# Kernel tuning notes

Measured on AMD Instinct MI355X. Metric: run time of the kernel, lower is better.

The kernel has to match this reference:

```python
import jax, jax.numpy as jnp
from jax import lax
import numpy as np

N, C, T, V, P, O = 32, 64, 300, 25, 3, 128
STRIDE = 2
EPS = 1e-5


def setup_inputs() -> dict:
    key = jax.random.key(0)
    ks = jax.random.split(key, 8)
    x = jax.random.normal(ks[0], (N, C, T, V), jnp.float32)
    A_parts = jax.random.uniform(ks[1], (P, V, V), jnp.float32)
    edge_importance = jnp.ones((P,), jnp.float32)
    gcn_w = jax.random.normal(ks[2], (O, C), jnp.float32) * 0.05
    gcn_b = jax.random.normal(ks[3], (O,), jnp.float32) * 0.05
    tcn_w = jax.random.normal(ks[4], (O, O, 9, 1), jnp.float32) * 0.02
    tcn_b = jax.random.normal(ks[5], (O,), jnp.float32) * 0.05
    bn_gamma = jnp.ones((O,), jnp.float32)
    bn_beta = jnp.zeros((O,), jnp.float32)
    res_w = jax.random.normal(ks[6], (O, C), jnp.float32) * 0.05
    res_b = jax.random.normal(ks[7], (O,), jnp.float32) * 0.05
    return {"x": x, "A_parts": A_parts, "edge_importance": edge_importance,
            "gcn_w": gcn_w, "gcn_b": gcn_b, "tcn_w": tcn_w, "tcn_b": tcn_b,
            "bn_gamma": bn_gamma, "bn_beta": bn_beta, "res_w": res_w, "res_b": res_b}


def reference(x, A_parts, edge_importance, gcn_w, gcn_b, tcn_w, tcn_b,
              bn_gamma, bn_beta, res_w, res_b):
    # Fused P-partition aggregation: sum_p (ei_p * A_p) applied once.
    A_sum = jnp.einsum('pvw,p->vw', A_parts, edge_importance)  # [V, V]
    agg = jnp.einsum('nctv,vw->nctw', x, A_sum)                # [N, C, T, V]
    # 1x1 gcn conv == channel matmul
    x_gcn = jnp.einsum('nctv,oc->notv', agg, gcn_w) + gcn_b[None, :, None, None]
    # temporal conv: kernel (9,1), stride (2,1), pad (4,0)
    x_tcn = lax.conv_general_dilated(
        x_gcn, tcn_w, window_strides=(STRIDE, 1), padding=((4, 4), (0, 0)),
        dimension_numbers=('NCHW', 'OIHW', 'NCHW'))
    x_tcn = x_tcn + tcn_b[None, :, None, None]
    # BatchNorm (training mode: batch statistics, biased variance)
    mean = jnp.mean(x_tcn, axis=(0, 2, 3), keepdims=True)
    var = jnp.var(x_tcn, axis=(0, 2, 3), keepdims=True)
    x_bn = (x_tcn - mean) * lax.rsqrt(var + EPS)
    x_bn = x_bn * bn_gamma[None, :, None, None] + bn_beta[None, :, None, None]
    # residual: 1x1 conv, stride (2,1) == temporal subsample + channel matmul
    x_sub = x[:, :, ::STRIDE, :]
    res = jnp.einsum('nctv,oc->notv', x_sub, res_w) + res_b[None, :, None, None]
    return jax.nn.relu(x_bn + res)
```

## Files before the change

kernel.cpp:

```cpp
#include <hip/hip_runtime.h>
#include <hip/hip_bf16.h>

typedef unsigned short u16;
typedef unsigned int   u32;

#define NB 32
#define CC 64
#define TT 300
#define VV 25
#define OO 128
#define TO 150
#define KT 9
#define MM 7500
#define MT 59
#define M2 3750

typedef short s8v  __attribute__((ext_vector_type(8)));
typedef float f4v  __attribute__((ext_vector_type(4)));
typedef u16  h4v  __attribute__((ext_vector_type(4)));
typedef u16  h8v  __attribute__((ext_vector_type(8)));

__device__ __forceinline__ float b2f(u16 u){
  union { u32 i; float f; } c; c.i = ((u32)u) << 16; return c.f;
}
__device__ __forceinline__ u16 f2b(float f){
  __hip_bfloat16 h = __float2bfloat16(f);
  return *reinterpret_cast<u16*>(&h);
}
__device__ __forceinline__ void async16(const void* g, void* l){
  __builtin_amdgcn_global_load_lds((const __attribute__((address_space(1))) u32*)g,
                                   (__attribute__((address_space(3))) u32*)l, 16, 0, 0);
}

__global__ __launch_bounds__(256) void k_prep(const float* __restrict__ Ap, const float* __restrict__ ei,
                                              const float* __restrict__ tw, const float* __restrict__ gw,
                                              const float* __restrict__ rw,
                                              float* __restrict__ Asum, float* __restrict__ zbuf,
                                              u16* __restrict__ Wq2, u16* __restrict__ gwb,
                                              u16* __restrict__ rwb){
  int idx = blockIdx.x * 256 + threadIdx.x;
  if (idx < VV*VV){
    float s = 0.f;
    for (int p = 0; p < 3; ++p) s += ei[p] * Ap[p*VV*VV + idx];
    Asum[idx] = s;
  }
  if (idx >= 640 && idx < 768) zbuf[idx - 640] = 0.f;
  int w = idx - 1024;
  if (w >= 0 && w < 18*OO*64){
    int kc = w >> 13;
    int r  = w & 8191;
    int o  = r >> 6;
    int j  = r & 63;
    int k  = kc >> 1;
    int i  = (kc & 1)*64 + j;
    Wq2[w] = f2b(tw[o*(OO*KT) + i*KT + k]);
  }
  int w2 = idx - 148480;
  if (w2 >= 0 && w2 < OO*CC) gwb[w2] = f2b(gw[w2]);
  int w3 = idx - 156672;
  if (w3 >= 0 && w3 < OO*CC) rwb[w3] = f2b(rw[w3]);
}

__global__ __launch_bounds__(256, 4) void k_gcnm(const float* __restrict__ x, const float* __restrict__ Asum,
                                                 const u16* __restrict__ gwb, const float* __restrict__ gb,
                                                 u16* __restrict__ xg){
  __shared__ __align__(16) u16 A_lds[128*64];
  __shared__ __align__(16) u16 B_lds[128*64];
  int bx = blockIdx.x;
  int n  = bx / MT;
  int m0 = (bx % MT) * 128;
  int t0 = m0 / VV, r0 = m0 % VV;
  int tid = threadIdx.x;
  int lane = tid & 63, wv = tid >> 6;
  int wm = (wv & 1) * 64, wo = (wv >> 1) * 64;
  int lr = lane & 15, lq = lane >> 4;

  {
    const u32* g32 = (const u32*)gwb;
    u32* b32 = (u32*)B_lds;
    for (int s = tid; s < 4096; s += 256){
      int row = s >> 5, col = s & 31;
      int g = col >> 2, c2 = col & 3;
      b32[row*32 + ((g ^ (row & 7))*4 + c2)] = g32[s];
    }
  }

  s8v bfw[2];
  #pragma unroll
  for (int wt = 0; wt < 2; ++wt){
    u16 tmp[8];
    int w = lr + 16*wt;
    #pragma unroll
    for (int j = 0; j < 8; ++j){
      int v = lq*8 + j;
      tmp[j] = (w < VV && v < VV) ? f2b(Asum[v*VV + w]) : (u16)0;
    }
    bfw[wt] = *(s8v*)tmp;
  }

  #pragma unroll
  for (int tt = 0; tt < 7; ++tt){
    int tau = tt*4 + wv;
    int it = tau >> 2, ct = tau & 3;
    int t  = t0 + it;
    int c  = ct*16 + lr;
    const float* xp = x + ((size_t)(n*CC + c)*TT + t)*VV + lq*8;
    float4 xa = make_float4(0.f,0.f,0.f,0.f), xb = xa;
    float x24 = 0.f;
    if (t < TT){
      if (lq < 3){
        xa = *(const float4*)xp;
        xb = *(const float4*)(xp + 4);
      } else {
        x24 = xp[0];
      }
    }
    u16 pk[8];
    if (lq < 3){
      pk[0]=f2b(xa.x); pk[1]=f2b(xa.y); pk[2]=f2b(xa.z); pk[3]=f2b(xa.w);
      pk[4]=f2b(xb.x); pk[5]=f2b(xb.y); pk[6]=f2b(xb.z); pk[7]=f2b(xb.w);
    } else {
      pk[0]=f2b(x24); pk[1]=0; pk[2]=0; pk[3]=0; pk[4]=0; pk[5]=0; pk[6]=0; pk[7]=0;
    }
    s8v af = *(s8v*)pk;
    f4v d0 = (f4v)(0.f), d1 = (f4v)(0.f);
    d0 = __builtin_amdgcn_mfma_f32_16x16x32_bf16(af, bfw[0], d0, 0, 0, 0);
    d1 = __builtin_amdgcn_mfma_f32_16x16x32_bf16(af, bfw[1], d1, 0, 0, 0);
    int cb = ct*16 + lq*4;
    int g  = cb >> 3, co = cb & 7;
    int ml0 = it*VV + lr - r0;
    if (ml0 >= 0 && ml0 < 128){
      u16 q[4];
      #pragma unroll
      for (int rg = 0; rg < 4; ++rg) q[rg] = f2b(d0[rg]);
      *(h4v*)&A_lds[ml0*64 + ((g ^ (ml0 & 7))*8) + co] = *(h4v*)q;
    }
    int w1 = lr + 16;
    int ml1 = it*VV + w1 - r0;
    if (w1 < VV && ml1 >= 0 && ml1 < 128){
      u16 q[4];
      #pragma unroll
      for (int rg = 0; rg < 4; ++rg) q[rg] = f2b(d1[rg]);
      *(h4v*)&A_lds[ml1*64 + ((g ^ (ml1 & 7))*8) + co] = *(h4v*)q;
    }
  }
  __syncthreads();

  f4v acc[4][4];
  #pragma unroll
  for (int mi = 0; mi < 4; ++mi)
    #pragma unroll
    for (int ni = 0; ni < 4; ++ni) acc[mi][ni] = (f4v)(0.f);
  #pragma unroll
  for (int ks = 0; ks < 2; ++ks){
    int p = ((ks*4 + lq) ^ (lane & 7)) * 8;
    s8v af[4], bf[4];
    #pragma unroll
    for (int mi = 0; mi < 4; ++mi)
      af[mi] = *(const s8v*)&A_lds[(wm + mi*16 + lr)*64 + p];
    #pragma unroll
    for (int ni = 0; ni < 4; ++ni)
      bf[ni] = *(const s8v*)&B_lds[(wo + ni*16 + lr)*64 + p];
    #pragma unroll
    for (int mi = 0; mi < 4; ++mi)
      #pragma unroll
      for (int ni = 0; ni < 4; ++ni)
        acc[mi][ni] = __builtin_amdgcn_mfma_f32_16x16x32_bf16(af[mi], bf[ni], acc[mi][ni], 0, 0, 0);
  }

  float bias[4];
  #pragma unroll
  for (int ni = 0; ni < 4; ++ni) bias[ni] = gb[wo + ni*16 + lr];
  #pragma unroll
  for (int mi = 0; mi < 4; ++mi){
    int mr = m0 + wm + mi*16 + lq*4;
    #pragma unroll
    for (int ni = 0; ni < 4; ++ni){
      int o = wo + ni*16 + lr;
      #pragma unroll
      for (int rg = 0; rg < 4; ++rg){
        int m = mr + rg;
        if (m < MM)
          xg[((size_t)n*MM + m)*OO + o] = f2b(acc[mi][ni][rg] + bias[ni]);
      }
    }
  }
}

__global__ __launch_bounds__(256) void k_tcnm(const u16* __restrict__ xg, const u16* __restrict__ Wq2,
                                              const float* __restrict__ tb, const u16* __restrict__ zbuf,
                                              u16* __restrict__ xt, float* __restrict__ psum,
                                              float* __restrict__ psq){
  __shared__ __align__(16) u16 A_lds[128*64];
  __shared__ __align__(16) u16 B_lds[128*64];
  __shared__ float sredS[4][64];
  __shared__ float sredQ[4][64];
  int bx = blockIdx.x;
  int n  = bx / 30;
  int m0 = (bx % 30) * 128;
  int tid = threadIdx.x;
  int lane = tid & 63, wv = tid >> 6;
  int wm = (wv & 1) * 64, wo = (wv >> 1) * 64;
  int lr = lane & 15, lq = lane >> 4;

  int rlow = tid >> 3;
  int gsrc = (tid & 7) ^ (rlow & 7);
  int tid16 = tid * 16;
  int  tbse[4], vr[4]; bool vm[4];
  #pragma unroll
  for (int it = 0; it < 4; ++it){
    int m = m0 + it*32 + rlow;
    vm[it] = (m < M2);
    int t2 = m / VV, v = m - t2*VV;
    tbse[it] = 2*t2 - 4;
    vr[it] = v;
  }
  size_t basen = (size_t)n*MM*OO + (size_t)gsrc*8;

  f4v acc[4][4];
  #pragma unroll
  for (int mi = 0; mi < 4; ++mi)
    #pragma unroll
    for (int ni = 0; ni < 4; ++ni) acc[mi][ni] = (f4v)(0.f);

  for (int kc = 0; kc < 18; ++kc){
    int k  = kc >> 1;
    int i0 = (kc & 1) * 64;
    const u16* wbase = Wq2 + kc*8192;
    #pragma unroll
    for (int it = 0; it < 4; ++it){
      int t = tbse[it] + k;
      const u16* ga = (vm[it] && t >= 0 && t < TT)
                      ? xg + basen + (size_t)(t*VV + vr[it])*OO + i0
                      : zbuf;
      async16(ga, (char*)A_lds + it*4096 + tid16);
      async16(wbase + ((it*32 + rlow)*64 + gsrc*8), (char*)B_lds + it*4096 + tid16);
    }
    __syncthreads();
    #pragma unroll
    for (int ks = 0; ks < 2; ++ks){
      int p = ((ks*4 + lq) ^ (lane & 7)) * 8;
      s8v af[4], bf[4];
      #pragma unroll
      for (int mi = 0; mi < 4; ++mi)
        af[mi] = *(const s8v*)&A_lds[(wm + mi*16 + lr)*64 + p];
      #pragma unroll
      for (int ni = 0; ni < 4; ++ni)
        bf[ni] = *(const s8v*)&B_lds[(wo + ni*16 + lr)*64 + p];
      #pragma unroll
      for (int mi = 0; mi < 4; ++mi)
        #pragma unroll
        for (int ni = 0; ni < 4; ++ni)
          acc[mi][ni] = __builtin_amdgcn_mfma_f32_16x16x32_bf16(af[mi], bf[ni], acc[mi][ni], 0, 0, 0);
    }
    __syncthreads();
  }

  float bias[4];
  #pragma unroll
  for (int ni = 0; ni < 4; ++ni) bias[ni] = tb[wo + ni*16 + lr];
  float sni[4] = {0.f,0.f,0.f,0.f}, qni[4] = {0.f,0.f,0.f,0.f};
  #pragma unroll
  for (int mi = 0; mi < 4; ++mi){
    int mr = m0 + wm + mi*16 + lq*4;
    #pragma unroll
    for (int ni = 0; ni < 4; ++ni){
      int o = wo + ni*16 + lr;
      #pragma unroll
      for (int rg = 0; rg < 4; ++rg){
        int m = mr + rg;
        if (m < M2){
          float val = acc[mi][ni][rg] + bias[ni];
          xt[((size_t)n*M2 + m)*OO + o] = f2b(val);
          sni[ni] += val;
          qni[ni] += val*val;
        }
      }
    }
  }
  #pragma unroll
  for (int ni = 0; ni < 4; ++ni){
    float s = sni[ni], q = qni[ni];
    s += __shfl_xor(s, 16); s += __shfl_xor(s, 32);
    q += __shfl_xor(q, 16); q += __shfl_xor(q, 32);
    if (lane < 16){
      sredS[wv][ni*16 + lane] = s;
      sredQ[wv][ni*16 + lane] = q;
    }
  }
  __syncthreads();
  if (tid < 128){
    int o = tid, base = (o >> 6)*2, lo = o & 63;
    psum[(size_t)bx*128 + o] = sredS[base][lo] + sredS[base+1][lo];
  } else {
    int o = tid - 128, base = (o >> 6)*2, lo = o & 63;
    psq [(size_t)bx*128 + o] = sredQ[base][lo] + sredQ[base+1][lo];
  }
}

__global__ __launch_bounds__(256) void k_stats2a(const float* __restrict__ psum, const float* __restrict__ psq,
                                                 float* __restrict__ ps2, float* __restrict__ pq2){
  __shared__ float bufS[256], bufQ[256];
  int tid = threadIdx.x, b = blockIdx.x;
  int o = tid & 127, h = tid >> 7;
  float s = 0.f, q = 0.f;
  for (int r = b*16 + h; r < b*16 + 16; r += 2){
    s += psum[(size_t)r*128 + o];
    q += psq [(size_t)r*128 + o];
  }
  bufS[tid] = s; bufQ[tid] = q;
  __syncthreads();
  if (tid < 128){
    ps2[(size_t)b*128 + o] = bufS[tid] + bufS[tid + 128];
    pq2[(size_t)b*128 + o] = bufQ[tid] + bufQ[tid + 128];
  }
}

__global__ __launch_bounds__(256) void k_stats2b(const float* __restrict__ ps2, const float* __restrict__ pq2,
                                                 const float* __restrict__ gamma, const float* __restrict__ beta,
                                                 float* __restrict__ stats){
  __shared__ float bufS[256], bufQ[256];
  int tid = threadIdx.x;
  int o = tid & 127, h = tid >> 7;
  float s = 0.f, q = 0.f;
  for (int b = h; b < 60; b += 2){
    s += ps2[(size_t)b*128 + o];
    q += pq2[(size_t)b*128 + o];
  }
  bufS[tid] = s; bufQ[tid] = q;
  __syncthreads();
  if (tid < 128){
    s = bufS[tid] + bufS[tid + 128];
    q = bufQ[tid] + bufQ[tid + 128];
    const float inv = 1.f / 120000.f;
    float mean = s * inv;
    float var  = q * inv - mean*mean;
    float sc = gamma[o] * rsqrtf(var + 1e-5f);
    stats[o]       = sc;
    stats[128 + o] = beta[o] - mean * sc;
  }
}

__global__ __launch_bounds__(256, 4) void k_resm(const float* __restrict__ x, const u16* __restrict__ rwb,
                                                 const float* __restrict__ rb, const u16* __restrict__ xt,
                                                 const float* __restrict__ stats, float* __restrict__ out){
  __shared__ __align__(16) u16 A_lds[128*64];
  __shared__ __align__(16) u16 B_lds[128*64];
  int bx = blockIdx.x;
  int n  = bx / 30;
  int m0 = (bx % 30) * 128;
  int t20 = m0 / VV, r0 = m0 % VV;
  int tid = threadIdx.x;
  int lane = tid & 63, wv = tid >> 6;
  int wm = (wv & 1) * 64, wo = (wv >> 1) * 64;
  int lr = lane & 15, lq = lane >> 4;

  {
    const u32* g32 = (const u32*)rwb;
    u32* b32 = (u32*)B_lds;
    for (int s = tid; s < 4096; s += 256){
      int row = s >> 5, col = s & 31;
      int g = col >> 2, c2 = col & 3;
      b32[row*32 + ((g ^ (row & 7))*4 + c2)] = g32[s];
    }
  }

  for (int task = tid; task < 8*7*VV; task += 256){
    int cg  = task / (7*VV);
    int rem = task - cg*(7*VV);
    int t2i = rem / VV, v = rem - t2i*VV;
    int t2 = t20 + t2i;
    int ml = t2i*VV + v - r0;
    if (ml >= 0 && ml < 128){
      u16 pk[8];
      if (t2 < TO){
        const float* xp = x + ((size_t)(n*CC + cg*8)*TT + 2*t2)*VV + v;
        #pragma unroll
        for (int cc = 0; cc < 8; ++cc) pk[cc] = f2b(xp[(size_t)cc*(TT*VV)]);
      } else {
        #pragma unroll
        for (int cc = 0; cc < 8; ++cc) pk[cc] = 0;
      }
      *(h8v*)&A_lds[ml*64 + ((cg ^ (ml & 7))*8)] = *(h8v*)pk;
    }
  }
  __syncthreads();

  f4v acc[4][4];
  #pragma unroll
  for (int mi = 0; mi < 4; ++mi)
    #pragma unroll
    for (int ni = 0; ni < 4; ++ni) acc[mi][ni] = (f4v)(0.f);
  #pragma unroll
  for (int ks = 0; ks < 2; ++ks){
    int p = ((ks*4 + lq) ^ (lane & 7)) * 8;
    s8v af[4], bf[4];
    #pragma unroll
    for (int mi = 0; mi < 4; ++mi)
      af[mi] = *(const s8v*)&A_lds[(wm + mi*16 + lr)*64 + p];
    #pragma unroll
    for (int ni = 0; ni < 4; ++ni)
      bf[ni] = *(const s8v*)&B_lds[(wo + ni*16 + lr)*64 + p];
    #pragma unroll
    for (int mi = 0; mi < 4; ++mi)
      #pragma unroll
      for (int ni = 0; ni < 4; ++ni)
        acc[mi][ni] = __builtin_amdgcn_mfma_f32_16x16x32_bf16(af[mi], bf[ni], acc[mi][ni], 0, 0, 0);
  }

  float sc[4], sb[4], rr[4];
  #pragma unroll
  for (int ni = 0; ni < 4; ++ni){
    int o = wo + ni*16 + lr;
    sc[ni] = stats[o]; sb[ni] = stats[128 + o]; rr[ni] = rb[o];
  }
  #pragma unroll
  for (int mi = 0; mi < 4; ++mi){
    int mb = m0 + wm + mi*16 + lq*4;
    #pragma unroll
    for (int ni = 0; ni < 4; ++ni){
      int o = wo + ni*16 + lr;
      size_t xb = ((size_t)n*M2 + mb)*OO + o;
      size_t ob = ((size_t)(n*OO + o))*M2 + mb;
      if (mb + 3 < M2){
        float r0_ = fmaxf(sc[ni]*b2f(xt[xb])        + sb[ni] + acc[mi][ni][0] + rr[ni], 0.f);
        float r1_ = fmaxf(sc[ni]*b2f(xt[xb + OO])   + sb[ni] + acc[mi][ni][1] + rr[ni], 0.f);
        float r2_ = fmaxf(sc[ni]*b2f(xt[xb + 2*OO]) + sb[ni] + acc[mi][ni][2] + rr[ni], 0.f);
        float r3_ = fmaxf(sc[ni]*b2f(xt[xb + 3*OO]) + sb[ni] + acc[mi][ni][3] + rr[ni], 0.f);
        *(float2*)&out[ob]     = make_float2(r0_, r1_);
        *(float2*)&out[ob + 2] = make_float2(r2_, r3_);
      } else {
        #pragma unroll
        for (int rg = 0; rg < 4; ++rg){
          int m = mb + rg;
          if (m < M2){
            float r = sc[ni]*b2f(xt[xb + (size_t)rg*OO]) + sb[ni] + acc[mi][ni][rg] + rr[ni];
            out[ob + rg] = fmaxf(r, 0.f);
          }
        }
      }
    }
  }
}

extern "C" void kernel_launch(void* const* d_in, const int* in_sizes, int n_in,
                              void* d_out, int out_size, void* d_ws, size_t ws_size,
                              hipStream_t stream) {
  const float* x     = (const float*)d_in[0];
  const float* Ap    = (const float*)d_in[1];
  const float* ei    = (const float*)d_in[2];
  const float* gw    = (const float*)d_in[3];
  const float* gb    = (const float*)d_in[4];
  const float* tw    = (const float*)d_in[5];
  const float* tb    = (const float*)d_in[6];
  const float* gamma = (const float*)d_in[7];
  const float* beta  = (const float*)d_in[8];
  const float* rw    = (const float*)d_in[9];
  const float* rb    = (const float*)d_in[10];
  float* out = (float*)d_out;

  char* ws = (char*)d_ws;
  float* Asum  = (float*)ws;
  float* zbuf  = (float*)(ws + 2560);
  u16*   Wq2   = (u16*)(ws + 4096);
  u16*   gwb   = (u16*)(ws + 299008);
  u16*   rwb   = (u16*)(ws + 315392);
  float* stats = (float*)(ws + 331776);
  float* psum  = (float*)(ws + 333824);
  float* psq   = (float*)(ws + 825344);
  float* ps2   = (float*)(ws + 1316864);
  float* pq2   = (float*)(ws + 1347584);
  u16*   xg    = (u16*)(ws + (2u<<20));
  u16*   xt    = (u16*)(ws + 63537152);

  k_prep   <<<dim3(644),    dim3(256), 0, stream>>>(Ap, ei, tw, gw, rw, Asum, zbuf, Wq2, gwb, rwb);
  k_gcnm   <<<dim3(NB*MT),  dim3(256), 0, stream>>>(x, Asum, gwb, gb, xg);
  k_tcnm   <<<dim3(NB*30),  dim3(256), 0, stream>>>(xg, Wq2, tb, (const u16*)zbuf, xt, psum, psq);
  k_stats2a<<<dim3(60),     dim3(256), 0, stream>>>(psum, psq, ps2, pq2);
  k_stats2b<<<dim3(1),      dim3(256), 0, stream>>>(ps2, pq2, gamma, beta, stats);
  k_resm   <<<dim3(NB*30),  dim3(256), 0, stream>>>(x, rwb, rb, xt, stats, out);
}
```

Before: 279.2 us.

## Double-buffer LDS tiles in temporal conv kernel to overlap loads with MFMA

Splits the A and B LDS tiles of the temporal-conv GEMM kernel into two buffers and prefetches the next k-chunk with async global-to-LDS copies while the current chunk is consumed by MFMAs. Explicit vmcnt waits let the in-flight prefetch stay outstanding across the barrier. This is meant to hide global load latency behind compute, at the cost of doubling LDS use (64KB per block), which may reduce how many blocks fit per CU.

```diff
diff --git a/kernel.cpp b/kernel.cpp
--- a/kernel.cpp
+++ b/kernel.cpp
@@ -191,8 +191,8 @@
                                               const float* __restrict__ tb, const u16* __restrict__ zbuf,
                                               u16* __restrict__ xt, float* __restrict__ psum,
                                               float* __restrict__ psq){
-  __shared__ __align__(16) u16 A_lds[128*64];
-  __shared__ __align__(16) u16 B_lds[128*64];
+  __shared__ __align__(16) u16 A_lds[2][128*64];
+  __shared__ __align__(16) u16 B_lds[2][128*64];
   __shared__ float sredS[4][64];
   __shared__ float sredQ[4][64];
   int bx = blockIdx.x;
@@ -223,37 +223,56 @@
     #pragma unroll
     for (int ni = 0; ni < 4; ++ni) acc[mi][ni] = (f4v)(0.f);
 
-  for (int kc = 0; kc < 18; ++kc){
+  auto stage = [&](int kc, int b){
     int k  = kc >> 1;
     int i0 = (kc & 1) * 64;
     const u16* wbase = Wq2 + kc*8192;
+    char* Ab = (char*)(&A_lds[b][0]);
+    char* Bb = (char*)(&B_lds[b][0]);
     #pragma unroll
     for (int it = 0; it < 4; ++it){
       int t = tbse[it] + k;
       const u16* ga = (vm[it] && t >= 0 && t < TT)
                       ? xg + basen + (size_t)(t*VV + vr[it])*OO + i0
                       : zbuf;
-      async16(ga, (char*)A_lds + it*4096 + tid16);
-      async16(wbase + ((it*32 + rlow)*64 + gsrc*8), (char*)B_lds + it*4096 + tid16);
-    }
-    __syncthreads();
+      async16(ga, Ab + it*4096 + tid16);
+      async16(wbase + ((it*32 + rlow)*64 + gsrc*8), Bb + it*4096 + tid16);
+    }
+  };
+
+  stage(0, 0);
+  for (int kc = 0; kc < 18; ++kc){
+    int cur = kc & 1;
+    if (kc < 17){
+      stage(kc + 1, cur ^ 1);
+      asm volatile("s_waitcnt vmcnt(8)" ::: "memory");
+    } else {
+      asm volatile("s_waitcnt vmcnt(0)" ::: "memory");
+    }
+    __builtin_amdgcn_s_barrier();
+    asm volatile("" ::: "memory");
+
+    const u16* Ac = &A_lds[cur][0];
+    const u16* Bc = &B_lds[cur][0];
     #pragma unroll
     for (int ks = 0; ks < 2; ++ks){
       int p = ((ks*4 + lq) ^ (lane & 7)) * 8;
       s8v af[4], bf[4];
       #pragma unroll
       for (int mi = 0; mi < 4; ++mi)
-        af[mi] = *(const s8v*)&A_lds[(wm + mi*16 + lr)*64 + p];
+        af[mi] = *(const s8v*)&Ac[(wm + mi*16 + lr)*64 + p];
       #pragma unroll
       for (int ni = 0; ni < 4; ++ni)
-        bf[ni] = *(const s8v*)&B_lds[(wo + ni*16 + lr)*64 + p];
+        bf[ni] = *(const s8v*)&Bc[(wo + ni*16 + lr)*64 + p];
       #pragma unroll
       for (int mi = 0; mi < 4; ++mi)
         #pragma unroll
         for (int ni = 0; ni < 4; ++ni)
           acc[mi][ni] = __builtin_amdgcn_mfma_f32_16x16x32_bf16(af[mi], bf[ni], acc[mi][ni], 0, 0, 0);
     }
-    __syncthreads();
+    asm volatile("s_waitcnt lgkmcnt(0)" ::: "memory");
+    __builtin_amdgcn_s_barrier();
+    asm volatile("" ::: "memory");
   }
 
   float bias[4];
```

After: 269.7 us. 3.4% less time.
